# Optimization experiments

Measured on AMD Instinct MI355X. Metric: run time of the kernel, lower is better.

Reference implementation:

```python
import jax, jax.numpy as jnp
import numpy as np

N_ENV = 100000
D_PS = 512
N_SPECIES = 4
N_SUPPORT = 256
N_STRUCT = 1000
ZETA = 2


def setup_inputs() -> dict:
    key = jax.random.key(0)
    k1, k2, k3, k4, k5 = jax.random.split(key, 5)
    power_spectrum = jax.random.normal(k1, (N_ENV, D_PS), dtype=jnp.float32)
    sp = jax.random.normal(k2, (N_SPECIES, N_SUPPORT, D_PS), dtype=jnp.float32)
    # CosineKernel asserts support points are unit-norm
    support_points = sp / jnp.linalg.norm(sp, axis=-1, keepdims=True)
    weights = jax.random.normal(k3, (N_SPECIES, 1, N_SUPPORT), dtype=jnp.float32)
    all_species = jax.random.randint(k4, (N_ENV,), 0, N_SPECIES, dtype=jnp.int64)
    structure_ids = jnp.sort(jax.random.randint(k5, (N_ENV,), 0, N_STRUCT, dtype=jnp.int64))
    return {
        "power_spectrum": power_spectrum,
        "support_points": support_points,
        "weights": weights,
        "all_species": all_species,
        "structure_ids": structure_ids,
    }


def reference(power_spectrum, support_points, weights, all_species, structure_ids):
    # Normalize each environment's power spectrum (CosineKernel)
    ps = power_spectrum / jnp.linalg.norm(power_spectrum, axis=1, keepdims=True)
    # Kernel of every environment against every species' support set: [N, S, M]
    k = jnp.einsum("nd,smd->nsm", ps, support_points) ** ZETA
    # Per-row energy contribution for each species: k @ weights[s].T -> [N, S]
    contrib = jnp.einsum("nsm,sm->ns", k, weights[:, 0, :])
    # Species masking: each row only contributes through its own species' kernel
    onehot = jax.nn.one_hot(all_species, N_SPECIES, dtype=contrib.dtype)  # [N, S]
    per_row = jnp.sum(contrib * onehot, axis=1)  # [N]
    # Segmented sum over structures (equivalent to looping over structures_slices)
    energy = jax.ops.segment_sum(per_row, structure_ids, num_segments=N_STRUCT)
    return energy[:, None]  # [n_structures, 1]
```

## Files before the change

### kernel.cpp

```cpp
#include <hip/hip_runtime.h>
#include <hip/hip_bf16.h>


constexpr int kNEnv     = 100000;
constexpr int kDPS      = 512;
constexpr int kNSpecies = 4;
constexpr int kNSupport = 256;
constexpr int kCap      = 32768;

constexpr int BN = 128;
constexpr int BM = 128;
constexpr int BK = 32;
constexpr int LDSS = 40;

typedef __attribute__((ext_vector_type(8))) short short8;
typedef __attribute__((ext_vector_type(4))) float f32x4;

__global__ void scatter_kernel(const int* __restrict__ species, const int* __restrict__ sid,
                               int* __restrict__ cnt, int* __restrict__ perm,
                               int* __restrict__ sidp) {
  __shared__ int lcnt[kNSpecies];
  __shared__ int lbase[kNSpecies];
  int t = threadIdx.x;
  if (t < kNSpecies) lcnt[t] = 0;
  __syncthreads();
  int i = blockIdx.x * 256 + t;
  bool v = i < kNEnv;
  int s = 0, r = 0, g = 0;
  if (v) { s = species[i]; r = atomicAdd(&lcnt[s], 1); g = sid[i]; }
  __syncthreads();
  if (t < kNSpecies) lbase[t] = lcnt[t] ? atomicAdd(&cnt[t], lcnt[t]) : 0;
  __syncthreads();
  if (v) {
    int d = s * kCap + lbase[s] + r;
    perm[d] = i;
    sidp[d] = g;
  }
}

__device__ inline short8 pack_bf16x8(const float4& a, const float4& b) {
  union { short8 v; __hip_bfloat162 h[4]; } u;
  u.h[0] = __float22bfloat162_rn({a.x, a.y});
  u.h[1] = __float22bfloat162_rn({a.z, a.w});
  u.h[2] = __float22bfloat162_rn({b.x, b.y});
  u.h[3] = __float22bfloat162_rn({b.z, b.w});
  return u.v;
}

__global__ __launch_bounds__(256) void gap_gemm_kernel(
    const float* __restrict__ ps, const float* __restrict__ sp,
    const float* __restrict__ w, const int* __restrict__ cnt,
    const int* __restrict__ perm, const int* __restrict__ sidp,
    float* __restrict__ energy) {
  const int s     = blockIdx.z;
  const int count = min(cnt[s], kCap);
  const int tile0 = blockIdx.x * BN;
  if (tile0 >= count) return;
  const int m0    = blockIdx.y * BM;

  __shared__ short a_sh[BN * LDSS];
  __shared__ short b_sh[BM * LDSS];
  __shared__ float red[4][64];
  __shared__ float sqs[2][BN];

  const int tid  = threadIdx.x;
  const int wv   = tid >> 6;
  const int lane = tid & 63;

  const int st_r = tid & 127;
  const int st_p = tid >> 7;

  const int ge   = tile0 + st_r;
  const int arow = perm[s * kCap + (ge < count ? ge : count - 1)];
  const float* a_src = ps + (size_t)arow * kDPS + st_p * 16;
  const float* b_src = sp + ((size_t)s * kNSupport + m0 + st_r) * kDPS + st_p * 16;
  const float* w_s   = w + s * kNSupport;

  const int wv_e = (wv & 1) * 64;
  const int wv_m = (wv >> 1) * 64;
  const int l15  = lane & 15;
  const int lq   = lane >> 4;

  float wgt[4];
  #pragma unroll
  for (int fj = 0; fj < 4; ++fj) wgt[fj] = w_s[m0 + wv_m + fj * 16 + l15];

  f32x4 acc[4][4];
  #pragma unroll
  for (int i = 0; i < 4; ++i)
    #pragma unroll
    for (int j = 0; j < 4; ++j) acc[i][j] = (f32x4)0.f;

  float sqsum = 0.f;

  float4 va[4], vb[4];
  #pragma unroll
  for (int j = 0; j < 4; ++j) {
    va[j] = *(const float4*)(a_src + j * 4);
    vb[j] = *(const float4*)(b_src + j * 4);
  }

  for (int k0 = 0; k0 < kDPS; k0 += BK) {
    __syncthreads();
    #pragma unroll
    for (int j = 0; j < 4; ++j)
      sqsum += va[j].x * va[j].x + va[j].y * va[j].y + va[j].z * va[j].z + va[j].w * va[j].w;
    {
      short* ap = &a_sh[st_r * LDSS + st_p * 16];
      *(short8*)(ap)     = pack_bf16x8(va[0], va[1]);
      *(short8*)(ap + 8) = pack_bf16x8(va[2], va[3]);
      short* bp = &b_sh[st_r * LDSS + st_p * 16];
      *(short8*)(bp)     = pack_bf16x8(vb[0], vb[1]);
      *(short8*)(bp + 8) = pack_bf16x8(vb[2], vb[3]);
    }
    __syncthreads();
    if (k0 + BK < kDPS) {
      #pragma unroll
      for (int j = 0; j < 4; ++j) {
        va[j] = *(const float4*)(a_src + k0 + BK + j * 4);
        vb[j] = *(const float4*)(b_src + k0 + BK + j * 4);
      }
    }
    short8 af[4], bf[4];
    #pragma unroll
    for (int fi = 0; fi < 4; ++fi)
      af[fi] = *(const short8*)&a_sh[(wv_e + fi * 16 + l15) * LDSS + lq * 8];
    #pragma unroll
    for (int fj = 0; fj < 4; ++fj)
      bf[fj] = *(const short8*)&b_sh[(wv_m + fj * 16 + l15) * LDSS + lq * 8];
    #pragma unroll
    for (int fi = 0; fi < 4; ++fi)
      #pragma unroll
      for (int fj = 0; fj < 4; ++fj)
        acc[fi][fj] = __builtin_amdgcn_mfma_f32_16x16x32_bf16(af[fi], bf[fj], acc[fi][fj], 0, 0, 0);
  }

  sqs[st_p][st_r] = sqsum;

  #pragma unroll
  for (int fi = 0; fi < 4; ++fi) {
    #pragma unroll
    for (int r = 0; r < 4; ++r) {
      float p = 0.f;
      #pragma unroll
      for (int fj = 0; fj < 4; ++fj) {
        float c = acc[fi][fj][r];
        p += c * c * wgt[fj];
      }
      p += __shfl_xor(p, 1, 64);
      p += __shfl_xor(p, 2, 64);
      p += __shfl_xor(p, 4, 64);
      p += __shfl_xor(p, 8, 64);
      if (l15 == 0) red[wv][fi * 16 + lq * 4 + r] = p;
    }
  }
  __syncthreads();
  if (tid < BN) {
    int h = tid >> 6, el = tid & 63;
    int row = h * 64 + el;
    float v = red[h][el] + red[h + 2][el];
    int g = tile0 + row;
    if (g < count) {
      float inv = 1.0f / (sqs[0][row] + sqs[1][row]);
      atomicAdd(&energy[sidp[s * kCap + g]], v * inv);
    }
  }
}

extern "C" void kernel_launch(void* const* d_in, const int* in_sizes, int n_in,
                              void* d_out, int out_size, void* d_ws, size_t ws_size,
                              hipStream_t stream) {
  const float* ps      = (const float*)d_in[0];
  const float* sp      = (const float*)d_in[1];
  const float* w       = (const float*)d_in[2];
  const int*   species = (const int*)d_in[3];
  const int*   sid     = (const int*)d_in[4];
  float* energy = (float*)d_out;

  char* wsb = (char*)d_ws;
  int* cnt  = (int*)wsb;
  int* perm = (int*)(wsb + 256);
  int* sidp = (int*)(wsb + 256 + 4 * kCap * sizeof(int));

  hipMemsetAsync(cnt, 0, 16, stream);
  hipMemsetAsync(energy, 0, out_size * sizeof(float), stream);

  scatter_kernel<<<(kNEnv + 255) / 256, 256, 0, stream>>>(species, sid, cnt, perm, sidp);

  dim3 grid(kCap / BN, kNSupport / BM, kNSpecies);
  gap_gemm_kernel<<<grid, 256, 0, stream>>>(ps, sp, w, cnt, perm, sidp, energy);
}
```

Baseline: 404.8 us.

## Pre-convert inputs to bf16 and load GEMM tiles via async global-to-LDS

Adds a conversion kernel that writes bf16 copies of the power spectrum and support points and precomputes inverse squared norms once. The GEMM then pulls tiles with global_load_lds directly into XOR-swizzled LDS with BK=64, so each input element is read and converted once per pass instead of per M-tile in fp32. The trade-off is an extra kernel and roughly 100 MB of workspace. The async path drops the register prefetch overlap, and the old path is kept as a fallback when the workspace is too small.

```diff
diff --git a/kernel.cpp b/kernel.cpp
--- a/kernel.cpp
+++ b/kernel.cpp
@@ -10,11 +10,24 @@
 
 constexpr int BN = 128;
 constexpr int BM = 128;
-constexpr int BK = 32;
-constexpr int LDSS = 40;
 
 typedef __attribute__((ext_vector_type(8))) short short8;
 typedef __attribute__((ext_vector_type(4))) float f32x4;
+
+__device__ __forceinline__ short8 pack_bf16x8(const float4& a, const float4& b) {
+  union { short8 v; __hip_bfloat162 h[4]; } u;
+  u.h[0] = __float22bfloat162_rn({a.x, a.y});
+  u.h[1] = __float22bfloat162_rn({a.z, a.w});
+  u.h[2] = __float22bfloat162_rn({b.x, b.y});
+  u.h[3] = __float22bfloat162_rn({b.z, b.w});
+  return u.v;
+}
+
+__device__ __forceinline__ void async16(const short* g, short* l) {
+  __builtin_amdgcn_global_load_lds(
+      (const __attribute__((address_space(1))) void*)g,
+      (__attribute__((address_space(3))) void*)l, 16, 0, 0);
+}
 
 __global__ void scatter_kernel(const int* __restrict__ species, const int* __restrict__ sid,
                                int* __restrict__ cnt, int* __restrict__ perm,
@@ -38,16 +51,140 @@
   }
 }
 
-__device__ inline short8 pack_bf16x8(const float4& a, const float4& b) {
-  union { short8 v; __hip_bfloat162 h[4]; } u;
-  u.h[0] = __float22bfloat162_rn({a.x, a.y});
-  u.h[1] = __float22bfloat162_rn({a.z, a.w});
-  u.h[2] = __float22bfloat162_rn({b.x, b.y});
-  u.h[3] = __float22bfloat162_rn({b.z, b.w});
-  return u.v;
-}
-
-__global__ __launch_bounds__(256) void gap_gemm_kernel(
+__global__ __launch_bounds__(256) void convert_kernel(
+    const float* __restrict__ ps, const float* __restrict__ sp,
+    short* __restrict__ a_bf, short* __restrict__ sp_bf, float* __restrict__ inv_sq) {
+  const int b = blockIdx.x, wv = threadIdx.x >> 6, lane = threadIdx.x & 63;
+  if (b < kNEnv / 4) {
+    int row = b * 4 + wv;
+    const float4* src = (const float4*)(ps + (size_t)row * kDPS) + lane * 2;
+    float4 x = src[0], y = src[1];
+    float s = x.x * x.x + x.y * x.y + x.z * x.z + x.w * x.w
+            + y.x * y.x + y.y * y.y + y.z * y.z + y.w * y.w;
+    *(short8*)(a_bf + (size_t)row * kDPS + lane * 8) = pack_bf16x8(x, y);
+    #pragma unroll
+    for (int off = 1; off < 64; off <<= 1) s += __shfl_xor(s, off, 64);
+    if (lane == 0) inv_sq[row] = 1.0f / s;
+  } else {
+    int row = (b - kNEnv / 4) * 4 + wv;
+    const float4* src = (const float4*)(sp + (size_t)row * kDPS) + lane * 2;
+    *(short8*)(sp_bf + (size_t)row * kDPS + lane * 8) = pack_bf16x8(src[0], src[1]);
+  }
+}
+
+__global__ __launch_bounds__(256) void gap_gemm_async(
+    const short* __restrict__ a_bf, const short* __restrict__ sp_bf,
+    const float* __restrict__ w, const int* __restrict__ cnt,
+    const int* __restrict__ perm, const int* __restrict__ sidp,
+    const float* __restrict__ inv_sq, float* __restrict__ energy) {
+  const int s     = blockIdx.z;
+  const int count = min(cnt[s], kCap);
+  const int tile0 = blockIdx.x * BN;
+  if (tile0 >= count) return;
+  const int m0    = blockIdx.y * BM;
+
+  __shared__ short a_sh[BN * 64];
+  __shared__ short b_sh[BM * 64];
+  __shared__ float red[4][64];
+  __shared__ int   prm[BN];
+
+  const int tid  = threadIdx.x;
+  const int wv   = tid >> 6;
+  const int lane = tid & 63;
+
+  if (tid < BN) {
+    int ge = tile0 + tid;
+    prm[tid] = perm[s * kCap + (ge < count ? ge : count - 1)];
+  }
+  __syncthreads();
+
+  const int srow   = lane >> 3;
+  const int schunk = (lane & 7) ^ srow;
+  const short* gA[4];
+  const short* gB[4];
+  #pragma unroll
+  for (int j = 0; j < 4; ++j) {
+    int r = j * 32 + wv * 8 + srow;
+    gA[j] = a_bf + (size_t)prm[r] * kDPS + schunk * 8;
+    gB[j] = sp_bf + ((size_t)(s * kNSupport + m0 + r)) * kDPS + schunk * 8;
+  }
+
+  const int wv_e = (wv & 1) * 64;
+  const int wv_m = (wv >> 1) * 64;
+  const int l15  = lane & 15;
+  const int lq   = lane >> 4;
+
+  const float* w_s = w + s * kNSupport;
+  float wgt[4];
+  #pragma unroll
+  for (int fj = 0; fj < 4; ++fj) wgt[fj] = w_s[m0 + wv_m + fj * 16 + l15];
+
+  f32x4 acc[4][4];
+  #pragma unroll
+  for (int i = 0; i < 4; ++i)
+    #pragma unroll
+    for (int j = 0; j < 4; ++j) acc[i][j] = (f32x4)0.f;
+
+  for (int k0 = 0; k0 < kDPS; k0 += 64) {
+    __syncthreads();
+    #pragma unroll
+    for (int j = 0; j < 4; ++j) {
+      short* base_a = &a_sh[(j * 4 + wv) * 512];
+      short* base_b = &b_sh[(j * 4 + wv) * 512];
+      async16(gA[j] + k0, base_a);
+      async16(gB[j] + k0, base_b);
+    }
+    __syncthreads();
+    #pragma unroll
+    for (int ks = 0; ks < 2; ++ks) {
+      short8 af[4], bfr[4];
+      #pragma unroll
+      for (int f = 0; f < 4; ++f) {
+        int rowA = wv_e + f * 16 + l15;
+        af[f]  = *(const short8*)&a_sh[rowA * 64 + (((ks * 4 + lq) ^ (rowA & 7)) * 8)];
+        int rowB = wv_m + f * 16 + l15;
+        bfr[f] = *(const short8*)&b_sh[rowB * 64 + (((ks * 4 + lq) ^ (rowB & 7)) * 8)];
+      }
+      #pragma unroll
+      for (int fi = 0; fi < 4; ++fi)
+        #pragma unroll
+        for (int fj = 0; fj < 4; ++fj)
+          acc[fi][fj] = __builtin_amdgcn_mfma_f32_16x16x32_bf16(af[fi], bfr[fj], acc[fi][fj], 0, 0, 0);
+    }
+  }
+
+  #pragma unroll
+  for (int fi = 0; fi < 4; ++fi) {
+    #pragma unroll
+    for (int r = 0; r < 4; ++r) {
+      float p = 0.f;
+      #pragma unroll
+      for (int fj = 0; fj < 4; ++fj) {
+        float c = acc[fi][fj][r];
+        p += c * c * wgt[fj];
+      }
+      p += __shfl_xor(p, 1, 64);
+      p += __shfl_xor(p, 2, 64);
+      p += __shfl_xor(p, 4, 64);
+      p += __shfl_xor(p, 8, 64);
+      if (l15 == 0) red[wv][fi * 16 + lq * 4 + r] = p;
+    }
+  }
+  __syncthreads();
+  if (tid < BN) {
+    int h = tid >> 6, el = tid & 63;
+    int row = h * 64 + el;
+    float v = red[h][el] + red[h + 2][el];
+    int g = tile0 + row;
+    if (g < count) {
+      int env = prm[row];
+      atomicAdd(&energy[sidp[s * kCap + g]], v * inv_sq[env]);
+    }
+  }
+}
+
+constexpr int LDSS = 40;
+__global__ __launch_bounds__(256) void gap_gemm_r2(
     const float* __restrict__ ps, const float* __restrict__ sp,
     const float* __restrict__ w, const int* __restrict__ cnt,
     const int* __restrict__ perm, const int* __restrict__ sidp,
@@ -66,7 +203,6 @@
   const int tid  = threadIdx.x;
   const int wv   = tid >> 6;
   const int lane = tid & 63;
-
   const int st_r = tid & 127;
   const int st_p = tid >> 7;
 
@@ -92,7 +228,6 @@
     for (int j = 0; j < 4; ++j) acc[i][j] = (f32x4)0.f;
 
   float sqsum = 0.f;
-
   float4 va[4], vb[4];
   #pragma unroll
   for (int j = 0; j < 4; ++j) {
@@ -100,7 +235,7 @@
     vb[j] = *(const float4*)(b_src + j * 4);
   }
 
-  for (int k0 = 0; k0 < kDPS; k0 += BK) {
+  for (int k0 = 0; k0 < kDPS; k0 += 32) {
     __syncthreads();
     #pragma unroll
     for (int j = 0; j < 4; ++j)
@@ -114,29 +249,28 @@
       *(short8*)(bp + 8) = pack_bf16x8(vb[2], vb[3]);
     }
     __syncthreads();
-    if (k0 + BK < kDPS) {
+    if (k0 + 32 < kDPS) {
       #pragma unroll
       for (int j = 0; j < 4; ++j) {
-        va[j] = *(const float4*)(a_src + k0 + BK + j * 4);
-        vb[j] = *(const float4*)(b_src + k0 + BK + j * 4);
+        va[j] = *(const float4*)(a_src + k0 + 32 + j * 4);
+        vb[j] = *(const float4*)(b_src + k0 + 32 + j * 4);
       }
     }
-    short8 af[4], bf[4];
+    short8 af[4], bfr[4];
     #pragma unroll
     for (int fi = 0; fi < 4; ++fi)
       af[fi] = *(const short8*)&a_sh[(wv_e + fi * 16 + l15) * LDSS + lq * 8];
     #pragma unroll
     for (int fj = 0; fj < 4; ++fj)
-      bf[fj] = *(const short8*)&b_sh[(wv_m + fj * 16 + l15) * LDSS + lq * 8];
+      bfr[fj] = *(const short8*)&b_sh[(wv_m + fj * 16 + l15) * LDSS + lq * 8];
     #pragma unroll
     for (int fi = 0; fi < 4; ++fi)
       #pragma unroll
       for (int fj = 0; fj < 4; ++fj)
-        acc[fi][fj] = __builtin_amdgcn_mfma_f32_16x16x32_bf16(af[fi], bf[fj], acc[fi][fj], 0, 0, 0);
+        acc[fi][fj] = __builtin_amdgcn_mfma_f32_16x16x32_bf16(af[fi], bfr[fj], acc[fi][fj], 0, 0, 0);
   }
 
   sqs[st_p][st_r] = sqsum;
-
   #pragma unroll
   for (int fi = 0; fi < 4; ++fi) {
     #pragma unroll
@@ -178,9 +312,14 @@
   float* energy = (float*)d_out;
 
   char* wsb = (char*)d_ws;
-  int* cnt  = (int*)wsb;
-  int* perm = (int*)(wsb + 256);
-  int* sidp = (int*)(wsb + 256 + 4 * kCap * sizeof(int));
+  size_t off = 0;
+  int* cnt  = (int*)(wsb + off); off += 256;
+  int* perm = (int*)(wsb + off); off += (size_t)kNSpecies * kCap * 4;
+  int* sidp = (int*)(wsb + off); off += (size_t)kNSpecies * kCap * 4;
+  float* inv_sq = (float*)(wsb + off); off += (size_t)kNEnv * 4; off = (off + 255) & ~255ull;
+  short* sp_bf  = (short*)(wsb + off); off += (size_t)kNSpecies * kNSupport * kDPS * 2; off = (off + 255) & ~255ull;
+  short* a_bf   = (short*)(wsb + off);
+  size_t need = off + (size_t)kNEnv * kDPS * 2;
 
   hipMemsetAsync(cnt, 0, 16, stream);
   hipMemsetAsync(energy, 0, out_size * sizeof(float), stream);
@@ -188,5 +327,11 @@
   scatter_kernel<<<(kNEnv + 255) / 256, 256, 0, stream>>>(species, sid, cnt, perm, sidp);
 
   dim3 grid(kCap / BN, kNSupport / BM, kNSpecies);
-  gap_gemm_kernel<<<grid, 256, 0, stream>>>(ps, sp, w, cnt, perm, sidp, energy);
-}
+  if (ws_size >= need) {
+    convert_kernel<<<kNEnv / 4 + (kNSpecies * kNSupport) / 4, 256, 0, stream>>>(
+        ps, sp, a_bf, sp_bf, inv_sq);
+    gap_gemm_async<<<grid, 256, 0, stream>>>(a_bf, sp_bf, w, cnt, perm, sidp, inv_sq, energy);
+  } else {
+    gap_gemm_r2<<<grid, 256, 0, stream>>>(ps, sp, w, cnt, perm, sidp, energy);
+  }
+}
```

After: 406.0 us. About the same (+0.3%).

## Cover all support points per block, pre-convert supports to bf16, double-buffer LDS

Applied to the files above, without the earlier changes.

Each block now takes 64 environment rows against all 256 support points of a species. Before, 128x128 tiles made every environment row get read and converted twice, once per half of the support set. A separate kernel converts the support points to bf16 once, so the GEMM loads half as many bytes for B and skips converting them. Shared memory is double-buffered with one barrier per k-step, A is prefetched two steps ahead, and a launch bound asks for 3 blocks per CU. The cost is more shared memory per block, an extra kernel launch, and the B tile being re-read from global or L2 by more blocks.

```diff
diff --git a/kernel.cpp b/kernel.cpp
--- a/kernel.cpp
+++ b/kernel.cpp
@@ -8,13 +8,21 @@
 constexpr int kNSupport = 256;
 constexpr int kCap      = 32768;
 
-constexpr int BN = 128;
-constexpr int BM = 128;
-constexpr int BK = 32;
-constexpr int LDSS = 40;
+constexpr int BN    = 64;
+constexpr int BK    = 32;
+constexpr int KITER = kDPS / BK;
 
 typedef __attribute__((ext_vector_type(8))) short short8;
 typedef __attribute__((ext_vector_type(4))) float f32x4;
+
+__device__ __forceinline__ short8 pack_bf16x8(const float4& a, const float4& b) {
+  union { short8 v; __hip_bfloat162 h[4]; } u;
+  u.h[0] = __float22bfloat162_rn({a.x, a.y});
+  u.h[1] = __float22bfloat162_rn({a.z, a.w});
+  u.h[2] = __float22bfloat162_rn({b.x, b.y});
+  u.h[3] = __float22bfloat162_rn({b.z, b.w});
+  return u.v;
+}
 
 __global__ void scatter_kernel(const int* __restrict__ species, const int* __restrict__ sid,
                                int* __restrict__ cnt, int* __restrict__ perm,
@@ -38,52 +46,51 @@
   }
 }
 
-__device__ inline short8 pack_bf16x8(const float4& a, const float4& b) {
-  union { short8 v; __hip_bfloat162 h[4]; } u;
-  u.h[0] = __float22bfloat162_rn({a.x, a.y});
-  u.h[1] = __float22bfloat162_rn({a.z, a.w});
-  u.h[2] = __float22bfloat162_rn({b.x, b.y});
-  u.h[3] = __float22bfloat162_rn({b.z, b.w});
-  return u.v;
-}
-
-__global__ __launch_bounds__(256) void gap_gemm_kernel(
-    const float* __restrict__ ps, const float* __restrict__ sp,
+__global__ __launch_bounds__(256) void convert_sp_kernel(
+    const float* __restrict__ sp, short* __restrict__ sp_bf) {
+  size_t g = ((size_t)blockIdx.x * 256 + threadIdx.x) * 8;
+  float4 x = *(const float4*)(sp + g);
+  float4 y = *(const float4*)(sp + g + 4);
+  *(short8*)(sp_bf + g) = pack_bf16x8(x, y);
+}
+
+__global__ __launch_bounds__(256, 3) void gap_gemm_kernel(
+    const float* __restrict__ ps, const short* __restrict__ sp_bf,
     const float* __restrict__ w, const int* __restrict__ cnt,
     const int* __restrict__ perm, const int* __restrict__ sidp,
     float* __restrict__ energy) {
-  const int s     = blockIdx.z;
+  const int s     = blockIdx.y;
   const int count = min(cnt[s], kCap);
   const int tile0 = blockIdx.x * BN;
   if (tile0 >= count) return;
-  const int m0    = blockIdx.y * BM;
-
-  __shared__ short a_sh[BN * LDSS];
-  __shared__ short b_sh[BM * LDSS];
-  __shared__ float red[4][64];
-  __shared__ float sqs[2][BN];
+
+  __shared__ short a_fr[2][4 * BN * 8];
+  __shared__ short b_fr[2][4 * kNSupport * 8];
+  __shared__ float red[4][BN];
+  __shared__ float sqs[4][BN];
+  __shared__ int   prm[BN];
 
   const int tid  = threadIdx.x;
   const int wv   = tid >> 6;
   const int lane = tid & 63;
-
-  const int st_r = tid & 127;
-  const int st_p = tid >> 7;
-
-  const int ge   = tile0 + st_r;
-  const int arow = perm[s * kCap + (ge < count ? ge : count - 1)];
-  const float* a_src = ps + (size_t)arow * kDPS + st_p * 16;
-  const float* b_src = sp + ((size_t)s * kNSupport + m0 + st_r) * kDPS + st_p * 16;
-  const float* w_s   = w + s * kNSupport;
-
-  const int wv_e = (wv & 1) * 64;
-  const int wv_m = (wv >> 1) * 64;
   const int l15  = lane & 15;
   const int lq   = lane >> 4;
 
-  float wgt[4];
-  #pragma unroll
-  for (int fj = 0; fj < 4; ++fj) wgt[fj] = w_s[m0 + wv_m + fj * 16 + l15];
+  if (tid < BN) {
+    int ge = tile0 + tid;
+    prm[tid] = perm[s * kCap + (ge < count ? ge : count - 1)];
+  }
+  __syncthreads();
+
+  const int c = tid & 3;
+  const int r = tid >> 2;
+
+  const float* aptr = ps + (size_t)prm[r] * kDPS + c * 8;
+  const short* bbase = sp_bf + (size_t)s * kNSupport * kDPS + c * 8;
+  const short* bptr0 = bbase + (size_t)(r +   0) * kDPS;
+  const short* bptr1 = bbase + (size_t)(r +  64) * kDPS;
+  const short* bptr2 = bbase + (size_t)(r + 128) * kDPS;
+  const short* bptr3 = bbase + (size_t)(r + 192) * kDPS;
 
   f32x4 acc[4][4];
   #pragma unroll
@@ -91,79 +98,88 @@
     #pragma unroll
     for (int j = 0; j < 4; ++j) acc[i][j] = (f32x4)0.f;
 
-  float sqsum = 0.f;
-
-  float4 va[4], vb[4];
-  #pragma unroll
-  for (int j = 0; j < 4; ++j) {
-    va[j] = *(const float4*)(a_src + j * 4);
-    vb[j] = *(const float4*)(b_src + j * 4);
-  }
-
-  for (int k0 = 0; k0 < kDPS; k0 += BK) {
-    __syncthreads();
-    #pragma unroll
-    for (int j = 0; j < 4; ++j)
-      sqsum += va[j].x * va[j].x + va[j].y * va[j].y + va[j].z * va[j].z + va[j].w * va[j].w;
-    {
-      short* ap = &a_sh[st_r * LDSS + st_p * 16];
-      *(short8*)(ap)     = pack_bf16x8(va[0], va[1]);
-      *(short8*)(ap + 8) = pack_bf16x8(va[2], va[3]);
-      short* bp = &b_sh[st_r * LDSS + st_p * 16];
-      *(short8*)(bp)     = pack_bf16x8(vb[0], vb[1]);
-      *(short8*)(bp + 8) = pack_bf16x8(vb[2], vb[3]);
+  float sq = 0.f;
+
+  float4 apre[2][2];
+  uint4  bpre[4];
+  apre[0][0] = *(const float4*)(aptr + 0);
+  apre[0][1] = *(const float4*)(aptr + 4);
+  apre[1][0] = *(const float4*)(aptr + BK + 0);
+  apre[1][1] = *(const float4*)(aptr + BK + 4);
+  bpre[0] = *(const uint4*)(bptr0);
+  bpre[1] = *(const uint4*)(bptr1);
+  bpre[2] = *(const uint4*)(bptr2);
+  bpre[3] = *(const uint4*)(bptr3);
+
+  #pragma unroll 2
+  for (int i = 0; i < KITER; ++i) {
+    const int buf = i & 1;
+    float4 x = apre[buf][0], y = apre[buf][1];
+    sq += x.x * x.x + x.y * x.y + x.z * x.z + x.w * x.w
+        + y.x * y.x + y.y * y.y + y.z * y.z + y.w * y.w;
+    *(short8*)&a_fr[buf][(c * BN + r) * 8] = pack_bf16x8(x, y);
+    *(uint4*)&b_fr[buf][(c * kNSupport + r +   0) * 8] = bpre[0];
+    *(uint4*)&b_fr[buf][(c * kNSupport + r +  64) * 8] = bpre[1];
+    *(uint4*)&b_fr[buf][(c * kNSupport + r + 128) * 8] = bpre[2];
+    *(uint4*)&b_fr[buf][(c * kNSupport + r + 192) * 8] = bpre[3];
+    if (i + 2 < KITER) {
+      int k2 = (i + 2) * BK;
+      apre[buf][0] = *(const float4*)(aptr + k2 + 0);
+      apre[buf][1] = *(const float4*)(aptr + k2 + 4);
+    }
+    if (i + 1 < KITER) {
+      int k1 = (i + 1) * BK;
+      bpre[0] = *(const uint4*)(bptr0 + k1);
+      bpre[1] = *(const uint4*)(bptr1 + k1);
+      bpre[2] = *(const uint4*)(bptr2 + k1);
+      bpre[3] = *(const uint4*)(bptr3 + k1);
     }
     __syncthreads();
-    if (k0 + BK < kDPS) {
-      #pragma unroll
-      for (int j = 0; j < 4; ++j) {
-        va[j] = *(const float4*)(a_src + k0 + BK + j * 4);
-        vb[j] = *(const float4*)(b_src + k0 + BK + j * 4);
-      }
-    }
-    short8 af[4], bf[4];
-    #pragma unroll
-    for (int fi = 0; fi < 4; ++fi)
-      af[fi] = *(const short8*)&a_sh[(wv_e + fi * 16 + l15) * LDSS + lq * 8];
-    #pragma unroll
-    for (int fj = 0; fj < 4; ++fj)
-      bf[fj] = *(const short8*)&b_sh[(wv_m + fj * 16 + l15) * LDSS + lq * 8];
+    short8 af[4], bf4[4];
+    #pragma unroll
+    for (int f = 0; f < 4; ++f)
+      af[f] = *(const short8*)&a_fr[buf][(lq * BN + f * 16 + l15) * 8];
+    #pragma unroll
+    for (int f = 0; f < 4; ++f)
+      bf4[f] = *(const short8*)&b_fr[buf][(lq * kNSupport + wv * 64 + f * 16 + l15) * 8];
     #pragma unroll
     for (int fi = 0; fi < 4; ++fi)
       #pragma unroll
       for (int fj = 0; fj < 4; ++fj)
-        acc[fi][fj] = __builtin_amdgcn_mfma_f32_16x16x32_bf16(af[fi], bf[fj], acc[fi][fj], 0, 0, 0);
-  }
-
-  sqs[st_p][st_r] = sqsum;
+        acc[fi][fj] = __builtin_amdgcn_mfma_f32_16x16x32_bf16(af[fi], bf4[fj], acc[fi][fj], 0, 0, 0);
+  }
+
+  sqs[c][r] = sq;
+
+  const float* w_s = w + s * kNSupport;
+  float wgt[4];
+  #pragma unroll
+  for (int fj = 0; fj < 4; ++fj) wgt[fj] = w_s[wv * 64 + fj * 16 + l15];
 
   #pragma unroll
   for (int fi = 0; fi < 4; ++fi) {
     #pragma unroll
-    for (int r = 0; r < 4; ++r) {
+    for (int rr = 0; rr < 4; ++rr) {
       float p = 0.f;
       #pragma unroll
       for (int fj = 0; fj < 4; ++fj) {
-        float c = acc[fi][fj][r];
-        p += c * c * wgt[fj];
+        float cv = acc[fi][fj][rr];
+        p += cv * cv * wgt[fj];
       }
       p += __shfl_xor(p, 1, 64);
       p += __shfl_xor(p, 2, 64);
       p += __shfl_xor(p, 4, 64);
       p += __shfl_xor(p, 8, 64);
-      if (l15 == 0) red[wv][fi * 16 + lq * 4 + r] = p;
+      if (l15 == 0) red[wv][fi * 16 + lq * 4 + rr] = p;
     }
   }
   __syncthreads();
   if (tid < BN) {
-    int h = tid >> 6, el = tid & 63;
-    int row = h * 64 + el;
-    float v = red[h][el] + red[h + 2][el];
-    int g = tile0 + row;
-    if (g < count) {
-      float inv = 1.0f / (sqs[0][row] + sqs[1][row]);
+    float v = red[0][tid] + red[1][tid] + red[2][tid] + red[3][tid];
+    float inv = 1.0f / (sqs[0][tid] + sqs[1][tid] + sqs[2][tid] + sqs[3][tid]);
+    int g = tile0 + tid;
+    if (g < count)
       atomicAdd(&energy[sidp[s * kCap + g]], v * inv);
-    }
   }
 }
 
@@ -178,15 +194,18 @@
   float* energy = (float*)d_out;
 
   char* wsb = (char*)d_ws;
-  int* cnt  = (int*)wsb;
-  int* perm = (int*)(wsb + 256);
-  int* sidp = (int*)(wsb + 256 + 4 * kCap * sizeof(int));
+  size_t off = 0;
+  int* cnt  = (int*)(wsb + off); off += 256;
+  int* perm = (int*)(wsb + off); off += (size_t)kNSpecies * kCap * 4;
+  int* sidp = (int*)(wsb + off); off += (size_t)kNSpecies * kCap * 4;
+  short* sp_bf = (short*)(wsb + off);
 
   hipMemsetAsync(cnt, 0, 16, stream);
   hipMemsetAsync(energy, 0, out_size * sizeof(float), stream);
 
   scatter_kernel<<<(kNEnv + 255) / 256, 256, 0, stream>>>(species, sid, cnt, perm, sidp);
-
-  dim3 grid(kCap / BN, kNSupport / BM, kNSpecies);
-  gap_gemm_kernel<<<grid, 256, 0, stream>>>(ps, sp, w, cnt, perm, sidp, energy);
-}
+  convert_sp_kernel<<<(kNSpecies * kNSupport * kDPS) / (256 * 8), 256, 0, stream>>>(sp, sp_bf);
+
+  dim3 grid(kCap / BN, kNSpecies);
+  gap_gemm_kernel<<<grid, 256, 0, stream>>>(ps, sp_bf, w, cnt, perm, sidp, energy);
+}
```

Result: slower. 436.0 us (+7.7%).
